# Performance work log

Hardware: AMD Instinct MI355X
Metric: run time of the kernel (lower is better)

The kernel has to match this reference:

```python
import jax, jax.numpy as jnp
import numpy as np

B, L, H, NH = 8, 1024, 1024, 16
HD = H // NH  # head_dim = 64
SCALE = HD ** -0.5


def setup_inputs() -> dict:
    key = jax.random.key(0)
    kx, kqkv, kw, kb = jax.random.split(key, 4)
    x = jax.random.normal(kx, (B, L, H), dtype=jnp.float32)
    # nn.Linear(H, 3H, bias=False): weight [3H, H]
    w_qkv = jax.random.normal(kqkv, (3 * H, H), dtype=jnp.float32) * (H ** -0.5)
    # out_proj: nn.Linear(H, H) with bias
    w_out = jax.random.normal(kw, (H, H), dtype=jnp.float32) * (H ** -0.5)
    b_out = jax.random.normal(kb, (H,), dtype=jnp.float32) * 0.01
    return {"x": x, "w_qkv": w_qkv, "w_out": w_out, "b_out": b_out}


def reference(x, w_qkv, w_out, b_out):
    # qkv projection: [B, L, 3H]
    qkv = jnp.einsum('bld,ed->ble', x, w_qkv)
    # rearrange 'b l (qkv h d) -> qkv b h l d'
    qkv = qkv.reshape(B, L, 3, NH, HD)
    q = qkv[:, :, 0].transpose(0, 2, 1, 3)  # [B, NH, L, HD]
    k = qkv[:, :, 1].transpose(0, 2, 1, 3)
    v = qkv[:, :, 2].transpose(0, 2, 1, 3)
    att = jnp.einsum('bhxd,bhyd->bhxy', q, k) * SCALE
    att = jax.nn.softmax(att, axis=-1)
    o = jnp.einsum('bhxy,bhyd->bhxd', att, v)  # [B, NH, L, HD]
    o = o.transpose(0, 2, 1, 3).reshape(B, L, H)
    return jnp.einsum('bld,ed->ble', o, w_out) + b_out
```

## Files before the change

kernel.cpp:

```cpp
#include <hip/hip_runtime.h>


typedef short s16x8 __attribute__((ext_vector_type(8)));
typedef float f32x4 __attribute__((ext_vector_type(4)));
typedef unsigned int u32x2 __attribute__((ext_vector_type(2)));
typedef unsigned int u32x4 __attribute__((ext_vector_type(4)));

__device__ __forceinline__ unsigned short f2bf(float f) {
    union { float f; unsigned u; } c; c.f = f;
    return (unsigned short)((c.u + 0x7FFFu + ((c.u >> 16) & 1u)) >> 16);
}
__device__ __forceinline__ unsigned pack2bf(float a, float b) {
    union { float f; unsigned u; } ca, cb; ca.f = a; cb.f = b;
    return __builtin_amdgcn_perm(cb.u + 0x8000u, ca.u + 0x8000u, 0x07060302u);
}

#define GLOAD_LDS(g, l) __builtin_amdgcn_global_load_lds( \
    (const __attribute__((address_space(1))) void*)(g),   \
    (__attribute__((address_space(3))) void*)(l), 16, 0, 0)

__global__ __launch_bounds__(256) void cvt3(
    const float* __restrict__ s0, unsigned short* __restrict__ d0, int n0,
    const float* __restrict__ s1, unsigned short* __restrict__ d1, int n1,
    const float* __restrict__ s2, unsigned short* __restrict__ d2, int n2)
{
    long i = ((long)blockIdx.x * 256 + threadIdx.x) * 8;
    const float* s; unsigned short* d; long off;
    if (i < n0)                  { s = s0; d = d0; off = i; }
    else if (i < (long)n0 + n1)  { s = s1; d = d1; off = i - n0; }
    else                         { s = s2; d = d2; off = i - n0 - n1; }
    f32x4 a = *(const f32x4*)(s + off);
    f32x4 b = *(const f32x4*)(s + off + 4);
    u32x4 r;
    r[0] = pack2bf(a[0], a[1]); r[1] = pack2bf(a[2], a[3]);
    r[2] = pack2bf(b[0], b[1]); r[3] = pack2bf(b[2], b[3]);
    *(u32x4*)(d + off) = r;
}

template<int EPI>
__global__ __launch_bounds__(256) void gemm16(
    const unsigned short* __restrict__ A, const unsigned short* __restrict__ Bm,
    unsigned short* __restrict__ Cq, unsigned short* __restrict__ Cv,
    float* __restrict__ Cf, const float* __restrict__ bias,
    int N, int K)
{
    __shared__ unsigned short As[128 * 64];
    __shared__ unsigned short Bs[128 * 64];
    const int tid = threadIdx.x, lane = tid & 63, wave = tid >> 6;
    const int quad = lane >> 4, l16 = lane & 15;
    const int wm = (wave >> 1) * 64, wn = (wave & 1) * 64;
    const int m0 = blockIdx.y * 128, n0 = blockIdx.x * 128;

    const int prow = tid >> 3;
    const int qch  = (tid & 7) ^ (prow & 7);
    const unsigned short* gA[4];
    const unsigned short* gB[4];
    #pragma unroll
    for (int c = 0; c < 4; ++c) {
        gA[c] = A + (size_t)(m0 + c * 32 + prow) * K + qch * 8;
        gB[c] = Bm + (size_t)(n0 + c * 32 + prow) * K + qch * 8;
    }
    const int sw = l16 & 7;

    f32x4 acc[4][4] = {};
    for (int k0 = 0; k0 < K; k0 += 64) {
        __syncthreads();
        #pragma unroll
        for (int c = 0; c < 4; ++c) {
            GLOAD_LDS(gA[c], As + (c * 256 + tid) * 8);
            GLOAD_LDS(gB[c], Bs + (c * 256 + tid) * 8);
            gA[c] += 64; gB[c] += 64;
        }
        __syncthreads();
        #pragma unroll
        for (int s = 0; s < 2; ++s) {
            s16x8 af[4], bf[4];
            const int pc = ((s * 4 + quad) ^ sw) * 8;
            #pragma unroll
            for (int i = 0; i < 4; ++i)
                af[i] = *(const s16x8*)(As + (wm + i * 16 + l16) * 64 + pc);
            #pragma unroll
            for (int j = 0; j < 4; ++j)
                bf[j] = *(const s16x8*)(Bs + (wn + j * 16 + l16) * 64 + pc);
            #pragma unroll
            for (int i = 0; i < 4; ++i)
                #pragma unroll
                for (int j = 0; j < 4; ++j)
                    acc[i][j] = __builtin_amdgcn_mfma_f32_16x16x32_bf16(af[i], bf[j], acc[i][j], 0, 0, 0);
        }
    }

    if (EPI == 1) {
        #pragma unroll
        for (int j = 0; j < 4; ++j) {
            int col = n0 + wn + j * 16 + l16;
            float bv = bias[col];
            #pragma unroll
            for (int i = 0; i < 4; ++i)
                #pragma unroll
                for (int r = 0; r < 4; ++r)
                    Cf[(size_t)(m0 + wm + i * 16 + quad * 4 + r) * N + col] = acc[i][j][r] + bv;
        }
    } else if (n0 < 2048) {
        const float qs = (n0 < 1024) ? 0.18033688f : 1.0f;
        #pragma unroll
        for (int j = 0; j < 4; ++j) {
            int col = n0 + wn + j * 16 + l16;
            #pragma unroll
            for (int i = 0; i < 4; ++i)
                #pragma unroll
                for (int r = 0; r < 4; ++r)
                    Cq[(size_t)(m0 + wm + i * 16 + quad * 4 + r) * 2048 + col] = f2bf(acc[i][j][r] * qs);
        }
    } else {
        #pragma unroll
        for (int j = 0; j < 4; ++j) {
            int dcol = n0 + wn + j * 16 + l16 - 2048;
            int hh = dcol >> 6, dd = dcol & 63;
            #pragma unroll
            for (int i = 0; i < 4; ++i) {
                int row = m0 + wm + i * 16 + quad * 4;
                int bb = row >> 10, l = row & 1023;
                u32x2 pw;
                pw[0] = pack2bf(acc[i][j][0], acc[i][j][1]);
                pw[1] = pack2bf(acc[i][j][2], acc[i][j][3]);
                *(u32x2*)(Cv + (size_t)((bb * 16 + hh) * 64 + dd) * 1024 + l) = pw;
            }
        }
    }
}

__global__ __launch_bounds__(256) void attn(
    const unsigned short* __restrict__ qk, const unsigned short* __restrict__ Vt,
    unsigned short* __restrict__ O)
{
    __shared__ unsigned short Ks[64 * 64];
    __shared__ unsigned short Vs[64 * 64];
    __shared__ unsigned short Ps[4][2][16 * 72];

    const int bh = blockIdx.y, b = bh >> 4, hh = bh & 15;
    const int q0 = blockIdx.x * 128;
    const int tid = threadIdx.x, lane = tid & 63, wave = tid >> 6;
    const int quad = lane >> 4, l16 = lane & 15;

    s16x8 qf[2][2];
    #pragma unroll
    for (int h = 0; h < 2; ++h) {
        const unsigned short* qrow =
            qk + (size_t)(b * 1024 + q0 + h * 64 + wave * 16 + l16) * 2048 + hh * 64;
        qf[h][0] = *(const s16x8*)(qrow + quad * 8);
        qf[h][1] = *(const s16x8*)(qrow + 32 + quad * 8);
    }

    const int rl = lane >> 3;
    const int qc = (lane & 7) ^ rl;
    const int g0 = wave * 2, g1 = g0 + 1;
    const unsigned short* srcK0 = qk + (size_t)(b * 1024 + g0 * 8 + rl) * 2048 + 1024 + hh * 64 + qc * 8;
    const unsigned short* srcK1 = qk + (size_t)(b * 1024 + g1 * 8 + rl) * 2048 + 1024 + hh * 64 + qc * 8;
    const unsigned short* srcV0 = Vt + (size_t)(bh * 64 + g0 * 8 + rl) * 1024 + qc * 8;
    const unsigned short* srcV1 = Vt + (size_t)(bh * 64 + g1 * 8 + rl) * 1024 + qc * 8;
    unsigned short* dK0 = Ks + g0 * 512 + lane * 8;
    unsigned short* dK1 = Ks + g1 * 512 + lane * 8;
    unsigned short* dV0 = Vs + g0 * 512 + lane * 8;
    unsigned short* dV1 = Vs + g1 * 512 + lane * 8;

    const int sw = l16 & 7;

    f32x4 Oacc[2][4] = {};
    float lsum[2] = {0.0f, 0.0f};

    for (int kv = 0; kv < 1024; kv += 64) {
        __syncthreads();
        GLOAD_LDS(srcK0, dK0);
        GLOAD_LDS(srcK1, dK1);
        GLOAD_LDS(srcV0, dV0);
        GLOAD_LDS(srcV1, dV1);
        srcK0 += (size_t)64 * 2048; srcK1 += (size_t)64 * 2048;
        srcV0 += 64; srcV1 += 64;
        __syncthreads();

        #pragma unroll
        for (int h = 0; h < 2; ++h) {
            unsigned short* Pw = &Ps[wave][h][0];
            f32x4 Sacc[4] = {};
            #pragma unroll
            for (int j = 0; j < 4; ++j) {
                #pragma unroll
                for (int s = 0; s < 2; ++s) {
                    s16x8 kf = *(const s16x8*)(Ks + (j * 16 + l16) * 64 + ((s * 4 + quad) ^ sw) * 8);
                    Sacc[j] = __builtin_amdgcn_mfma_f32_16x16x32_bf16(kf, qf[h][s], Sacc[j], 0, 0, 0);
                }
            }
            #pragma unroll
            for (int j = 0; j < 4; ++j) {
                float p0 = __builtin_amdgcn_exp2f(Sacc[j][0]);
                float p1 = __builtin_amdgcn_exp2f(Sacc[j][1]);
                float p2 = __builtin_amdgcn_exp2f(Sacc[j][2]);
                float p3 = __builtin_amdgcn_exp2f(Sacc[j][3]);
                lsum[h] += (p0 + p1) + (p2 + p3);
                u32x2 pw;
                pw[0] = pack2bf(p0, p1);
                pw[1] = pack2bf(p2, p3);
                *(u32x2*)(Pw + l16 * 72 + j * 16 + quad * 4) = pw;
            }
            asm volatile("s_waitcnt lgkmcnt(0)" ::: "memory");
            #pragma unroll
            for (int s = 0; s < 2; ++s) {
                s16x8 pf = *(const s16x8*)(Pw + l16 * 72 + s * 32 + quad * 8);
                #pragma unroll
                for (int j = 0; j < 4; ++j) {
                    s16x8 vf = *(const s16x8*)(Vs + (j * 16 + l16) * 64 + ((s * 4 + quad) ^ sw) * 8);
                    Oacc[h][j] = __builtin_amdgcn_mfma_f32_16x16x32_bf16(pf, vf, Oacc[h][j], 0, 0, 0);
                }
            }
        }
    }

    #pragma unroll
    for (int h = 0; h < 2; ++h) {
        float ls = lsum[h];
        ls += __shfl_xor(ls, 16, 64);
        ls += __shfl_xor(ls, 32, 64);
        float rinv[4];
        #pragma unroll
        for (int r = 0; r < 4; ++r)
            rinv[r] = 1.0f / __shfl(ls, quad * 4 + r, 64);
        #pragma unroll
        for (int j = 0; j < 4; ++j)
            #pragma unroll
            for (int r = 0; r < 4; ++r) {
                int row = q0 + h * 64 + wave * 16 + quad * 4 + r;
                int col = hh * 64 + j * 16 + l16;
                O[(size_t)(b * 1024 + row) * 1024 + col] = f2bf(Oacc[h][j][r] * rinv[r]);
            }
    }
}

extern "C" void kernel_launch(void* const* d_in, const int* in_sizes, int n_in,
                              void* d_out, int out_size, void* d_ws, size_t ws_size,
                              hipStream_t stream) {
    const float* x     = (const float*)d_in[0];
    const float* w_qkv = (const float*)d_in[1];
    const float* w_out = (const float*)d_in[2];
    const float* b_out = (const float*)d_in[3];
    float* out = (float*)d_out;

    const int nx = 8192 * 1024, nwq = 3072 * 1024, nwo = 1024 * 1024;
    unsigned short* xb  = (unsigned short*)d_ws;
    unsigned short* wqb = xb + nx;
    unsigned short* wob = wqb + nwq;
    unsigned short* qkb = wob + nwo;
    unsigned short* Vt  = qkb + (size_t)8192 * 2048;
    unsigned short* Ob  = xb;

    dim3 blk(256);
    cvt3<<<6144, blk, 0, stream>>>(x, xb, nx, w_qkv, wqb, nwq, w_out, wob, nwo);
    gemm16<0><<<dim3(24, 64), blk, 0, stream>>>(xb, wqb, qkb, Vt, nullptr, nullptr, 3072, 1024);
    attn<<<dim3(8, 128), blk, 0, stream>>>(qkb, Vt, Ob);
    gemm16<1><<<dim3(8, 64), blk, 0, stream>>>(Ob, wob, nullptr, nullptr, out, b_out, 1024, 1024);
}
```

Measured before the change: 236.5 us.

## Keep softmax probabilities in registers by permuting K row layout in LDS

Removes the per-wave LDS scratch buffer used to transpose P between the QK^T and PV MFMAs. Instead, K rows are loaded into shared memory in a permuted order so the S accumulator layout directly matches the A-operand layout needed by the PV MFMA, letting packed bf16 probabilities be fed from registers. This eliminates LDS writes, a wait, and LDS reads per tile, at the cost of a more intricate load address mapping whose correctness depends on the permutation matching the MFMA layouts.

```diff
diff --git a/kernel.cpp b/kernel.cpp
--- a/kernel.cpp
+++ b/kernel.cpp
@@ -136,7 +136,6 @@
 {
     __shared__ unsigned short Ks[64 * 64];
     __shared__ unsigned short Vs[64 * 64];
-    __shared__ unsigned short Ps[4][2][16 * 72];
 
     const int bh = blockIdx.y, b = bh >> 4, hh = bh & 15;
     const int q0 = blockIdx.x * 128;
@@ -154,15 +153,18 @@
 
     const int rl = lane >> 3;
     const int qc = (lane & 7) ^ rl;
-    const int g0 = wave * 2, g1 = g0 + 1;
-    const unsigned short* srcK0 = qk + (size_t)(b * 1024 + g0 * 8 + rl) * 2048 + 1024 + hh * 64 + qc * 8;
-    const unsigned short* srcK1 = qk + (size_t)(b * 1024 + g1 * 8 + rl) * 2048 + 1024 + hh * 64 + qc * 8;
-    const unsigned short* srcV0 = Vt + (size_t)(bh * 64 + g0 * 8 + rl) * 1024 + qc * 8;
-    const unsigned short* srcV1 = Vt + (size_t)(bh * 64 + g1 * 8 + rl) * 1024 + qc * 8;
-    unsigned short* dK0 = Ks + g0 * 512 + lane * 8;
-    unsigned short* dK1 = Ks + g1 * 512 + lane * 8;
-    unsigned short* dV0 = Vs + g0 * 512 + lane * 8;
-    unsigned short* dV1 = Vs + g1 * 512 + lane * 8;
+    const int u0 = rl >> 2, r0 = rl & 3;
+    const int kvbase = 32 * (wave >> 1) + 4 * (wave & 1) + r0;
+    const int kv0 = kvbase + 8 * u0;
+    const int kv1 = kvbase + 8 * (2 + u0);
+    const unsigned short* srcK0 = qk + (size_t)(b * 1024 + kv0) * 2048 + 1024 + hh * 64 + qc * 8;
+    const unsigned short* srcK1 = qk + (size_t)(b * 1024 + kv1) * 2048 + 1024 + hh * 64 + qc * 8;
+    const unsigned short* srcV0 = Vt + (size_t)(bh * 64 + wave * 16 + rl) * 1024 + qc * 8;
+    const unsigned short* srcV1 = Vt + (size_t)(bh * 64 + wave * 16 + 8 + rl) * 1024 + qc * 8;
+    unsigned short* dK0 = Ks + (wave * 16 + rl) * 64 + (lane & 7) * 8;
+    unsigned short* dK1 = Ks + (wave * 16 + 8 + rl) * 64 + (lane & 7) * 8;
+    unsigned short* dV0 = Vs + (wave * 16 + rl) * 64 + (lane & 7) * 8;
+    unsigned short* dV1 = Vs + (wave * 16 + 8 + rl) * 64 + (lane & 7) * 8;
 
     const int sw = l16 & 7;
 
@@ -181,36 +183,37 @@
 
         #pragma unroll
         for (int h = 0; h < 2; ++h) {
-            unsigned short* Pw = &Ps[wave][h][0];
             f32x4 Sacc[4] = {};
             #pragma unroll
-            for (int j = 0; j < 4; ++j) {
+            for (int t = 0; t < 4; ++t) {
                 #pragma unroll
                 for (int s = 0; s < 2; ++s) {
-                    s16x8 kf = *(const s16x8*)(Ks + (j * 16 + l16) * 64 + ((s * 4 + quad) ^ sw) * 8);
-                    Sacc[j] = __builtin_amdgcn_mfma_f32_16x16x32_bf16(kf, qf[h][s], Sacc[j], 0, 0, 0);
+                    s16x8 kf = *(const s16x8*)(Ks + (t * 16 + l16) * 64 + ((s * 4 + quad) ^ sw) * 8);
+                    Sacc[t] = __builtin_amdgcn_mfma_f32_16x16x32_bf16(kf, qf[h][s], Sacc[t], 0, 0, 0);
                 }
             }
-            #pragma unroll
-            for (int j = 0; j < 4; ++j) {
-                float p0 = __builtin_amdgcn_exp2f(Sacc[j][0]);
-                float p1 = __builtin_amdgcn_exp2f(Sacc[j][1]);
-                float p2 = __builtin_amdgcn_exp2f(Sacc[j][2]);
-                float p3 = __builtin_amdgcn_exp2f(Sacc[j][3]);
+            unsigned upw[4][2];
+            #pragma unroll
+            for (int t = 0; t < 4; ++t) {
+                float p0 = __builtin_amdgcn_exp2f(Sacc[t][0]);
+                float p1 = __builtin_amdgcn_exp2f(Sacc[t][1]);
+                float p2 = __builtin_amdgcn_exp2f(Sacc[t][2]);
+                float p3 = __builtin_amdgcn_exp2f(Sacc[t][3]);
                 lsum[h] += (p0 + p1) + (p2 + p3);
-                u32x2 pw;
-                pw[0] = pack2bf(p0, p1);
-                pw[1] = pack2bf(p2, p3);
-                *(u32x2*)(Pw + l16 * 72 + j * 16 + quad * 4) = pw;
-            }
-            asm volatile("s_waitcnt lgkmcnt(0)" ::: "memory");
+                upw[t][0] = pack2bf(p0, p1);
+                upw[t][1] = pack2bf(p2, p3);
+            }
             #pragma unroll
             for (int s = 0; s < 2; ++s) {
-                s16x8 pf = *(const s16x8*)(Pw + l16 * 72 + s * 32 + quad * 8);
-                #pragma unroll
-                for (int j = 0; j < 4; ++j) {
-                    s16x8 vf = *(const s16x8*)(Vs + (j * 16 + l16) * 64 + ((s * 4 + quad) ^ sw) * 8);
-                    Oacc[h][j] = __builtin_amdgcn_mfma_f32_16x16x32_bf16(pf, vf, Oacc[h][j], 0, 0, 0);
+                u32x4 aw;
+                aw[0] = upw[2 * s][0];     aw[1] = upw[2 * s][1];
+                aw[2] = upw[2 * s + 1][0]; aw[3] = upw[2 * s + 1][1];
+                s16x8 pf;
+                __builtin_memcpy(&pf, &aw, 16);
+                #pragma unroll
+                for (int jd = 0; jd < 4; ++jd) {
+                    s16x8 vf = *(const s16x8*)(Vs + (jd * 16 + l16) * 64 + ((s * 4 + quad) ^ sw) * 8);
+                    Oacc[h][jd] = __builtin_amdgcn_mfma_f32_16x16x32_bf16(pf, vf, Oacc[h][jd], 0, 0, 0);
                 }
             }
         }
```

After: 236.0 us. No clear change (-0.2%).
